# Performance work log

Measured on AMD Instinct MI355X. Metric: run time of the kernel, lower is better.

Reference implementation:

```python
import jax, jax.numpy as jnp
import numpy as np

IOU_THRESHOLD = 0.5
EPS = 1e-7  # ultralytics bbox_iou eps


def _bbox_iou_xywh(b1, b2):
    # b1, b2: broadcastable [..., 4] in (cx, cy, w, h) format (ultralytics default xywh=True)
    x1, y1, w1, h1 = b1[..., 0], b1[..., 1], b1[..., 2], b1[..., 3]
    x2, y2, w2, h2 = b2[..., 0], b2[..., 1], b2[..., 2], b2[..., 3]
    b1x1, b1x2 = x1 - w1 * 0.5, x1 + w1 * 0.5
    b1y1, b1y2 = y1 - h1 * 0.5, y1 + h1 * 0.5
    b2x1, b2x2 = x2 - w2 * 0.5, x2 + w2 * 0.5
    b2y1, b2y2 = y2 - h2 * 0.5, y2 + h2 * 0.5
    iw = jnp.clip(jnp.minimum(b1x2, b2x2) - jnp.maximum(b1x1, b2x1), 0.0)
    ih = jnp.clip(jnp.minimum(b1y2, b2y2) - jnp.maximum(b1y1, b2y1), 0.0)
    inter = iw * ih
    union = w1 * h1 + w2 * h2 - inter + EPS
    return inter / union


def setup_inputs() -> dict:
    key = jax.random.key(0)
    k1, k2, k3, k4, k5 = jax.random.split(key, 5)
    N, R, M, C = 2048, 10, 2048, 84
    xy = jax.random.uniform(k1, (N, 2), minval=0.0, maxval=1000.0)
    wh = jax.random.uniform(k2, (N, 2), minval=30.0, maxval=80.0)
    boxes = jnp.concatenate([xy, wh], axis=-1)                      # [N, 4] xywh
    pred = jnp.concatenate([boxes, jax.random.uniform(k3, (N, C - 4))], axis=-1)  # [N, C]
    # dropout runs: same boxes with ~1px jitter -> IoU > 0.5 guaranteed (realistic MC-dropout)
    dropout_preds = boxes[None, :, :] + jax.random.normal(k4, (R, M, 4))          # [R, M, 4]
    dropout_cls_confs = jax.nn.softmax(jax.random.normal(k5, (R, M, C)), axis=-1)  # [R, M, C]
    return {"pred": pred, "dropout_preds": dropout_preds, "dropout_cls_confs": dropout_cls_confs}


def reference(pred, dropout_preds, dropout_cls_confs):
    # pred: [N, C] (first 4 cols = xywh box); dropout_preds: [R, M, 4]; dropout_cls_confs: [R, M, C]
    R = dropout_preds.shape[0]
    iou = _bbox_iou_xywh(pred[:, None, None, :4], dropout_preds[None, :, :, :])  # [N, R, M]
    hit = iou > IOU_THRESHOLD                                                    # [N, R, M]
    matched = jnp.any(hit, axis=-1)                                              # [N, R]
    first_idx = jnp.argmax(hit, axis=-1)                                         # first j with iou>thr (torch break)
    # gather cls confidences of the first match per (pred, run): [N, R, C]
    conf = dropout_cls_confs[jnp.arange(R)[None, :], first_idx]
    # runs without a match contribute nothing to the entropy sum; p=1 -> -p*log(p)=0
    p = jnp.where(matched[..., None], conf, 1.0)
    entropy = -(p * jnp.log(p)).sum(axis=1)                                      # [N, C], sum over matched runs
    # faithful to torch: zero fallback row gives 0*log(0)=nan entropy
    entropy = jnp.where(jnp.any(matched, axis=1)[:, None], entropy, jnp.nan)
    sm = jax.nn.softmax(entropy, axis=-1)                                        # softmax over classes
    return (1.0 - sm).max(axis=-1)                                               # [N]
```

## Files before the change

kernel.cpp:

```cpp
#include <hip/hip_runtime.h>
#include <math.h>

#define NN 2048
#define RR 10
#define MM 2048
#define CC 84
#define IOU_THR 0.5f
#define IEPS 1e-7f

__global__ __launch_bounds__(256) void match_kernel(
    const float* __restrict__ pred,
    const float* __restrict__ dpreds,
    int* __restrict__ first_idx) {
  int wid = (blockIdx.x * blockDim.x + threadIdx.x) >> 6;
  int lane = threadIdx.x & 63;
  if (wid >= NN * RR) return;
  int n = wid / RR;
  int r = wid % RR;

  float4 pb = *reinterpret_cast<const float4*>(pred + (size_t)n * CC);
  float b1x1 = pb.x - pb.z * 0.5f, b1x2 = pb.x + pb.z * 0.5f;
  float b1y1 = pb.y - pb.w * 0.5f, b1y2 = pb.y + pb.w * 0.5f;
  float area1 = pb.z * pb.w;

  const float* dp = dpreds + (size_t)r * MM * 4;
  int found = -1;
  for (int m0 = 0; m0 < MM; m0 += 64) {
    int m = m0 + lane;
    float4 db = *reinterpret_cast<const float4*>(dp + (size_t)m * 4);
    float b2x1 = db.x - db.z * 0.5f, b2x2 = db.x + db.z * 0.5f;
    float b2y1 = db.y - db.w * 0.5f, b2y2 = db.y + db.w * 0.5f;
    float iw = fmaxf(fminf(b1x2, b2x2) - fmaxf(b1x1, b2x1), 0.0f);
    float ih = fmaxf(fminf(b1y2, b2y2) - fmaxf(b1y1, b2y1), 0.0f);
    float inter = iw * ih;
    float uni = area1 + db.z * db.w - inter + IEPS;
    float iou = inter / uni;
    unsigned long long bal = __ballot(iou > IOU_THR);
    if (bal) {
      found = m0 + (__ffsll((unsigned long long)bal) - 1);
      break;
    }
  }
  if (lane == 0) first_idx[wid] = found;
}

__global__ __launch_bounds__(256) void entropy_kernel(
    const float* __restrict__ confs,
    const int* __restrict__ first_idx,
    float* __restrict__ out) {
  int lane = threadIdx.x & 63;
  int n = blockIdx.x * (blockDim.x >> 6) + (threadIdx.x >> 6);
  if (n >= NN) return;

  int idxs[RR];
  bool anym = false;
#pragma unroll
  for (int r = 0; r < RR; ++r) {
    idxs[r] = first_idx[n * RR + r];
    anym = anym || (idxs[r] >= 0);
  }

  const bool has_hi = (lane + 64) < CC;
  float e0 = 0.0f, e1 = 0.0f;
#pragma unroll
  for (int r = 0; r < RR; ++r) {
    if (idxs[r] >= 0) {
      const float* row = confs + ((size_t)r * MM + (size_t)idxs[r]) * CC;
      float p0 = row[lane];
      e0 -= p0 * logf(p0);
      if (has_hi) {
        float p1 = row[lane + 64];
        e1 -= p1 * logf(p1);
      }
    }
  }

  float maxE = fmaxf(e0, has_hi ? e1 : -INFINITY);
  float minE = fminf(e0, has_hi ? e1 : INFINITY);
#pragma unroll
  for (int off = 32; off >= 1; off >>= 1) {
    maxE = fmaxf(maxE, __shfl_xor(maxE, off));
    minE = fminf(minE, __shfl_xor(minE, off));
  }
  float s = expf(e0 - maxE) + (has_hi ? expf(e1 - maxE) : 0.0f);
#pragma unroll
  for (int off = 32; off >= 1; off >>= 1) s += __shfl_xor(s, off);

  float result = anym ? (1.0f - expf(minE - maxE) / s) : nanf("");
  if (lane == 0) out[n] = result;
}

extern "C" void kernel_launch(void* const* d_in, const int* in_sizes, int n_in,
                              void* d_out, int out_size, void* d_ws, size_t ws_size,
                              hipStream_t stream) {
  const float* pred   = (const float*)d_in[0];
  const float* dpreds = (const float*)d_in[1];
  const float* confs  = (const float*)d_in[2];
  float* out = (float*)d_out;
  int* first_idx = (int*)d_ws;

  {
    int total_waves = NN * RR;
    int blocks = (total_waves * 64 + 255) / 256;
    match_kernel<<<blocks, 256, 0, stream>>>(pred, dpreds, first_idx);
  }
  {
    int blocks = (NN + 3) / 4;
    entropy_kernel<<<blocks, 256, 0, stream>>>(confs, first_idx, out);
  }
}
```

Baseline: 28.50 us.

## Unroll match scan by four, replace IoU division with multiply compare, use fast math

The match loop now handles 256 candidates per iteration, issuing four float4 loads and four ballots per step, and turns the IoU>0.5 test into the division-free comparison 3*inter > area2+area1+eps. The entropy kernel switches to the __logf/__expf intrinsics. The aim is to cut per-iteration latency and remove the divide, but a match near the start now costs four loads. The rearranged threshold and fast intrinsics can differ slightly from the reference at borderline IoU values and in the low bits of the entropy.

Result: faster. 23.10 us, median of 2 (-19.0%).

```diff
diff --git a/kernel.cpp b/kernel.cpp
--- a/kernel.cpp
+++ b/kernel.cpp
@@ -5,7 +5,6 @@
 #define RR 10
 #define MM 2048
 #define CC 84
-#define IOU_THR 0.5f
 #define IEPS 1e-7f
 
 __global__ __launch_bounds__(256) void match_kernel(
@@ -16,28 +15,46 @@
   int lane = threadIdx.x & 63;
   if (wid >= NN * RR) return;
   int n = wid / RR;
-  int r = wid % RR;
+  int r = wid - n * RR;
 
   float4 pb = *reinterpret_cast<const float4*>(pred + (size_t)n * CC);
-  float b1x1 = pb.x - pb.z * 0.5f, b1x2 = pb.x + pb.z * 0.5f;
-  float b1y1 = pb.y - pb.w * 0.5f, b1y2 = pb.y + pb.w * 0.5f;
-  float area1 = pb.z * pb.w;
+  const float b1x1 = fmaf(-0.5f, pb.z, pb.x), b1x2 = fmaf(0.5f, pb.z, pb.x);
+  const float b1y1 = fmaf(-0.5f, pb.w, pb.y), b1y2 = fmaf(0.5f, pb.w, pb.y);
+  const float a1e = pb.z * pb.w + IEPS;
 
-  const float* dp = dpreds + (size_t)r * MM * 4;
+  const float4* __restrict__ dp =
+      reinterpret_cast<const float4*>(dpreds + (size_t)r * MM * 4);
+
   int found = -1;
-  for (int m0 = 0; m0 < MM; m0 += 64) {
-    int m = m0 + lane;
-    float4 db = *reinterpret_cast<const float4*>(dp + (size_t)m * 4);
-    float b2x1 = db.x - db.z * 0.5f, b2x2 = db.x + db.z * 0.5f;
-    float b2y1 = db.y - db.w * 0.5f, b2y2 = db.y + db.w * 0.5f;
-    float iw = fmaxf(fminf(b1x2, b2x2) - fmaxf(b1x1, b2x1), 0.0f);
-    float ih = fmaxf(fminf(b1y2, b2y2) - fmaxf(b1y1, b2y1), 0.0f);
-    float inter = iw * ih;
-    float uni = area1 + db.z * db.w - inter + IEPS;
-    float iou = inter / uni;
-    unsigned long long bal = __ballot(iou > IOU_THR);
-    if (bal) {
-      found = m0 + (__ffsll((unsigned long long)bal) - 1);
+  for (int m0 = 0; m0 < MM; m0 += 256) {
+    float4 d0 = dp[m0 + lane];
+    float4 d1 = dp[m0 + 64 + lane];
+    float4 d2 = dp[m0 + 128 + lane];
+    float4 d3 = dp[m0 + 192 + lane];
+
+#define HIT(db, h)                                                          \
+    {                                                                       \
+      float x1 = fmaf(-0.5f, db.z, db.x), x2 = fmaf(0.5f, db.z, db.x);      \
+      float y1 = fmaf(-0.5f, db.w, db.y), y2 = fmaf(0.5f, db.w, db.y);      \
+      float iw = fmaxf(fminf(b1x2, x2) - fmaxf(b1x1, x1), 0.0f);            \
+      float ih = fmaxf(fminf(b1y2, y2) - fmaxf(b1y1, y1), 0.0f);            \
+      float inter = iw * ih;                                                \
+      float t = db.z * db.w + a1e;                       \
+      h = (3.0f * inter > t);                                               \
+    }
+    bool h0, h1, h2, h3;
+    HIT(d0, h0) HIT(d1, h1) HIT(d2, h2) HIT(d3, h3)
+#undef HIT
+
+    unsigned long long b0 = __ballot(h0);
+    unsigned long long b1 = __ballot(h1);
+    unsigned long long b2 = __ballot(h2);
+    unsigned long long b3 = __ballot(h3);
+    if (b0 | b1 | b2 | b3) {
+      if (b0)      found = m0 +       (__ffsll(b0) - 1);
+      else if (b1) found = m0 + 64  + (__ffsll(b1) - 1);
+      else if (b2) found = m0 + 128 + (__ffsll(b2) - 1);
+      else         found = m0 + 192 + (__ffsll(b3) - 1);
       break;
     }
   }
@@ -67,10 +84,10 @@
     if (idxs[r] >= 0) {
       const float* row = confs + ((size_t)r * MM + (size_t)idxs[r]) * CC;
       float p0 = row[lane];
-      e0 -= p0 * logf(p0);
+      e0 -= p0 * __logf(p0);
       if (has_hi) {
         float p1 = row[lane + 64];
-        e1 -= p1 * logf(p1);
+        e1 -= p1 * __logf(p1);
       }
     }
   }
@@ -82,11 +99,11 @@
     maxE = fmaxf(maxE, __shfl_xor(maxE, off));
     minE = fminf(minE, __shfl_xor(minE, off));
   }
-  float s = expf(e0 - maxE) + (has_hi ? expf(e1 - maxE) : 0.0f);
+  float s = __expf(e0 - maxE) + (has_hi ? __expf(e1 - maxE) : 0.0f);
 #pragma unroll
   for (int off = 32; off >= 1; off >>= 1) s += __shfl_xor(s, off);
 
-  float result = anym ? (1.0f - expf(minE - maxE) / s) : nanf("");
+  float result = anym ? (1.0f - __expf(minE - maxE) / s) : nanf("");
   if (lane == 0) out[n] = result;
 }
 
```

## Batch eight predictions per wave in IoU matching and drop the division

Applied to the files above, without the earlier changes.

Each wave in the match kernel now handles a group of 8 consecutive predictions for one dropout run instead of a single prediction. Every loaded dropout box is reused across all 8 predictions, and the scan exits only once all 8 have found a match. The IoU threshold test is rewritten as 3*inter > a1+a2+eps, which removes the per-element division. The next dropout tile is prefetched in a register, and the entropy kernel switches to fast __logf/__expf intrinsics. The trade-off is 8x fewer waves with more serial ballot and branch work per wave, which could hurt latency hiding.

Result: slower. 32.63 us (+14.5%).

```diff
diff --git a/kernel.cpp b/kernel.cpp
--- a/kernel.cpp
+++ b/kernel.cpp
@@ -5,43 +5,68 @@
 #define RR 10
 #define MM 2048
 #define CC 84
-#define IOU_THR 0.5f
+#define GG 8
 #define IEPS 1e-7f
 
 __global__ __launch_bounds__(256) void match_kernel(
     const float* __restrict__ pred,
     const float* __restrict__ dpreds,
     int* __restrict__ first_idx) {
+  const int NG = NN / GG;
   int wid = (blockIdx.x * blockDim.x + threadIdx.x) >> 6;
   int lane = threadIdx.x & 63;
-  if (wid >= NN * RR) return;
-  int n = wid / RR;
-  int r = wid % RR;
+  if (wid >= NG * RR) return;
+  int g = wid % NG;
+  int r = wid / NG;
+  int nb = g * GG;
 
-  float4 pb = *reinterpret_cast<const float4*>(pred + (size_t)n * CC);
-  float b1x1 = pb.x - pb.z * 0.5f, b1x2 = pb.x + pb.z * 0.5f;
-  float b1y1 = pb.y - pb.w * 0.5f, b1y2 = pb.y + pb.w * 0.5f;
-  float area1 = pb.z * pb.w;
+  float bx1[GG], bx2[GG], by1[GG], by2[GG], a1e[GG];
+#pragma unroll
+  for (int i = 0; i < GG; ++i) {
+    float4 pb = *reinterpret_cast<const float4*>(pred + (size_t)(nb + i) * CC);
+    bx1[i] = fmaf(-0.5f, pb.z, pb.x);
+    bx2[i] = fmaf(0.5f, pb.z, pb.x);
+    by1[i] = fmaf(-0.5f, pb.w, pb.y);
+    by2[i] = fmaf(0.5f, pb.w, pb.y);
+    a1e[i] = pb.z * pb.w + IEPS;
+  }
 
-  const float* dp = dpreds + (size_t)r * MM * 4;
-  int found = -1;
+  const float4* __restrict__ dp =
+      reinterpret_cast<const float4*>(dpreds + (size_t)r * MM * 4);
+
+  unsigned done = 0;
+  const unsigned ALL = (1u << GG) - 1;
+  float4 d = dp[lane];
   for (int m0 = 0; m0 < MM; m0 += 64) {
-    int m = m0 + lane;
-    float4 db = *reinterpret_cast<const float4*>(dp + (size_t)m * 4);
-    float b2x1 = db.x - db.z * 0.5f, b2x2 = db.x + db.z * 0.5f;
-    float b2y1 = db.y - db.w * 0.5f, b2y2 = db.y + db.w * 0.5f;
-    float iw = fmaxf(fminf(b1x2, b2x2) - fmaxf(b1x1, b2x1), 0.0f);
-    float ih = fmaxf(fminf(b1y2, b2y2) - fmaxf(b1y1, b2y1), 0.0f);
-    float inter = iw * ih;
-    float uni = area1 + db.z * db.w - inter + IEPS;
-    float iou = inter / uni;
-    unsigned long long bal = __ballot(iou > IOU_THR);
-    if (bal) {
-      found = m0 + (__ffsll((unsigned long long)bal) - 1);
-      break;
+    float4 dn = d;
+    if (m0 + 64 < MM) dn = dp[m0 + 64 + lane];
+
+    float x1 = fmaf(-0.5f, d.z, d.x), x2 = fmaf(0.5f, d.z, d.x);
+    float y1 = fmaf(-0.5f, d.w, d.y), y2 = fmaf(0.5f, d.w, d.y);
+    float a2 = d.z * d.w;
+
+#pragma unroll
+    for (int i = 0; i < GG; ++i) {
+      if (done & (1u << i)) continue;
+      float iw = fmaxf(fminf(bx2[i], x2) - fmaxf(bx1[i], x1), 0.0f);
+      float ih = fmaxf(fminf(by2[i], y2) - fmaxf(by1[i], y1), 0.0f);
+      float inter = iw * ih;
+      float t = a2 + a1e[i];
+      unsigned long long bal = __ballot(3.0f * inter > t);
+      if (bal) {
+        done |= (1u << i);
+        if (lane == 0)
+          first_idx[(size_t)(nb + i) * RR + r] = m0 + (__ffsll(bal) - 1);
+      }
     }
+    if (done == ALL) break;
+    d = dn;
   }
-  if (lane == 0) first_idx[wid] = found;
+  if (lane == 0) {
+#pragma unroll
+    for (int i = 0; i < GG; ++i)
+      if (!(done & (1u << i))) first_idx[(size_t)(nb + i) * RR + r] = -1;
+  }
 }
 
 __global__ __launch_bounds__(256) void entropy_kernel(
@@ -67,10 +92,10 @@
     if (idxs[r] >= 0) {
       const float* row = confs + ((size_t)r * MM + (size_t)idxs[r]) * CC;
       float p0 = row[lane];
-      e0 -= p0 * logf(p0);
+      e0 -= p0 * __logf(p0);
       if (has_hi) {
         float p1 = row[lane + 64];
-        e1 -= p1 * logf(p1);
+        e1 -= p1 * __logf(p1);
       }
     }
   }
@@ -82,11 +107,11 @@
     maxE = fmaxf(maxE, __shfl_xor(maxE, off));
     minE = fminf(minE, __shfl_xor(minE, off));
   }
-  float s = expf(e0 - maxE) + (has_hi ? expf(e1 - maxE) : 0.0f);
+  float s = __expf(e0 - maxE) + (has_hi ? __expf(e1 - maxE) : 0.0f);
 #pragma unroll
   for (int off = 32; off >= 1; off >>= 1) s += __shfl_xor(s, off);
 
-  float result = anym ? (1.0f - expf(minE - maxE) / s) : nanf("");
+  float result = anym ? (1.0f - __expf(minE - maxE) / s) : nanf("");
   if (lane == 0) out[n] = result;
 }
 
@@ -100,7 +125,7 @@
   int* first_idx = (int*)d_ws;
 
   {
-    int total_waves = NN * RR;
+    int total_waves = (NN / GG) * RR;
     int blocks = (total_waves * 64 + 255) / 256;
     match_kernel<<<blocks, 256, 0, stream>>>(pred, dpreds, first_idx);
   }
```
